# Performance work log

Hardware: AMD Instinct MI355X
Metric: run time of the kernel (lower is better)

Reference implementation:

```python
import jax, jax.numpy as jnp
import numpy as np

B, N_ST, N_SUB, WIN = 32, 8, 256, 2048


def setup_inputs() -> dict:
    key = jax.random.key(0)
    k1, k2 = jax.random.split(key)
    sel = jax.random.randint(k1, (B, WIN), 0, N_ST)
    schedule = jax.nn.one_hot(sel, N_ST, dtype=jnp.float32)
    # CSI: [B, n_stations, n_subcarriers, window]
    csi = jax.random.normal(k2, (B, N_ST, N_SUB, WIN), dtype=jnp.float32)
    return {"schedule": schedule, "csi": csi}


def reference(schedule, csi):
    # mask[b,t,s,w] = schedule[b,w,t]; out[b,s,w] = sum_t csi[b,t,s,w] * schedule[b,w,t]
    out = jnp.einsum('btsw,bwt->bsw', csi, schedule)
    return jnp.transpose(out, (0, 2, 1))
```

## Files before the change

kernel.cpp:

```cpp
#include <hip/hip_runtime.h>

constexpr int B     = 32;
constexpr int N_ST  = 8;
constexpr int N_SUB = 256;
constexpr int WIN   = 2048;

constexpr int TW  = 256;
constexpr int TS  = 16;
constexpr int STR = 260;

typedef float f4 __attribute__((ext_vector_type(4)));

__global__ __launch_bounds__(256)
void station_agg_kernel(const float* __restrict__ schedule,
                        const float* __restrict__ csi,
                        float* __restrict__ out)
{
    __shared__ float sched_t[N_ST][TW];
    __shared__ float tile2[TS * STR];

    const int s0 = blockIdx.x * TS;
    const int w0 = blockIdx.y * TW;
    const int b  = blockIdx.z;
    const int k  = threadIdx.x;
    const int wv = k >> 6;
    const int l  = k & 63;

    {
        const float* sp = schedule + ((size_t)b * WIN + w0 + k) * N_ST;
        const f4 a = *(const f4*)sp;
        const f4 c = *(const f4*)(sp + 4);
        sched_t[0][k] = a.x; sched_t[1][k] = a.y;
        sched_t[2][k] = a.z; sched_t[3][k] = a.w;
        sched_t[4][k] = c.x; sched_t[5][k] = c.y;
        sched_t[6][k] = c.z; sched_t[7][k] = c.w;
    }
    __syncthreads();

    f4 acc[4];
#pragma unroll
    for (int j = 0; j < 4; ++j) acc[j] = (f4)(0.0f);

    const size_t bbase = (size_t)b * N_ST * N_SUB * WIN;
#pragma unroll
    for (int t = 0; t < N_ST; ++t) {
        const f4 sv = *(const f4*)&sched_t[t][4 * l];
        const float* cp = csi + bbase
                        + ((size_t)t * N_SUB + (s0 + 4 * wv)) * WIN
                        + (w0 + 4 * l);
#pragma unroll
        for (int j = 0; j < 4; ++j) {
            const f4 c = __builtin_nontemporal_load((const f4*)(cp + (size_t)j * WIN));
            acc[j] += c * sv;
        }
    }

#pragma unroll
    for (int j = 0; j < 4; ++j)
        *(f4*)&tile2[(4 * wv + j) * STR + 4 * l] = acc[j];
    __syncthreads();

#pragma unroll
    for (int m = 0; m < 4; ++m) {
        const int wrow = 16 * wv + (l >> 2) + 64 * m;
        const int sl   = 4 * (l & 3);
        f4 o;
        o.x = tile2[(sl + 0) * STR + wrow];
        o.y = tile2[(sl + 1) * STR + wrow];
        o.z = tile2[(sl + 2) * STR + wrow];
        o.w = tile2[(sl + 3) * STR + wrow];
        __builtin_nontemporal_store(o,
            (f4*)(out + ((size_t)b * WIN + (w0 + wrow)) * N_SUB + (s0 + sl)));
    }
}

extern "C" void kernel_launch(void* const* d_in, const int* in_sizes, int n_in,
                              void* d_out, int out_size, void* d_ws, size_t ws_size,
                              hipStream_t stream) {
    const float* schedule = (const float*)d_in[0];
    const float* csi      = (const float*)d_in[1];
    float* out            = (float*)d_out;

    dim3 grid(N_SUB / TS, WIN / TW, B);
    dim3 block(256);
    station_agg_kernel<<<grid, block, 0, stream>>>(schedule, csi, out);
}
```

Baseline: 675.7 us.

## Batch CSI loads per half and drop LDS transpose for in-register stores

Groups the eight station loads into two batches of sixteen vector loads issued before any FMA, to raise memory-level parallelism. It also removes the shared-memory transpose tile and second barrier: each thread transposes its 4x4 accumulator block in registers and writes four 16-byte stores directly to the output. The cost is higher register pressure and less coalesced output writes, since each lane writes 16 bytes at stride N_SUB rather than forming contiguous rows across the wavefront. Output stores also change from nontemporal to regular.

```diff
diff --git a/kernel.cpp b/kernel.cpp
--- a/kernel.cpp
+++ b/kernel.cpp
@@ -7,7 +7,6 @@
 
 constexpr int TW  = 256;
 constexpr int TS  = 16;
-constexpr int STR = 260;
 
 typedef float f4 __attribute__((ext_vector_type(4)));
 
@@ -17,7 +16,6 @@
                         float* __restrict__ out)
 {
     __shared__ float sched_t[N_ST][TW];
-    __shared__ float tile2[TS * STR];
 
     const int s0 = blockIdx.x * TS;
     const int w0 = blockIdx.y * TW;
@@ -42,35 +40,45 @@
     for (int j = 0; j < 4; ++j) acc[j] = (f4)(0.0f);
 
     const size_t bbase = (size_t)b * N_ST * N_SUB * WIN;
+    const int    srow  = s0 + 4 * wv;
+    const int    wl    = w0 + 4 * l;
+
 #pragma unroll
-    for (int t = 0; t < N_ST; ++t) {
-        const f4 sv = *(const f4*)&sched_t[t][4 * l];
-        const float* cp = csi + bbase
-                        + ((size_t)t * N_SUB + (s0 + 4 * wv)) * WIN
-                        + (w0 + 4 * l);
+    for (int h = 0; h < 2; ++h) {
+        f4 cbuf[4][4];
+        f4 sv[4];
 #pragma unroll
-        for (int j = 0; j < 4; ++j) {
-            const f4 c = __builtin_nontemporal_load((const f4*)(cp + (size_t)j * WIN));
-            acc[j] += c * sv;
+        for (int tt = 0; tt < 4; ++tt) {
+            const int t = 4 * h + tt;
+            const float* cp = csi + bbase
+                            + ((size_t)t * N_SUB + srow) * WIN + wl;
+#pragma unroll
+            for (int j = 0; j < 4; ++j) {
+                cbuf[tt][j] = __builtin_nontemporal_load((const f4*)(cp + (size_t)j * WIN));
+            }
+        }
+#pragma unroll
+        for (int tt = 0; tt < 4; ++tt) {
+            sv[tt] = *(const f4*)&sched_t[4 * h + tt][4 * l];
+        }
+#pragma unroll
+        for (int tt = 0; tt < 4; ++tt) {
+#pragma unroll
+            for (int j = 0; j < 4; ++j) {
+                acc[j] += cbuf[tt][j] * sv[tt];
+            }
         }
     }
 
+    float* op = out + ((size_t)b * WIN + wl) * N_SUB + srow;
 #pragma unroll
-    for (int j = 0; j < 4; ++j)
-        *(f4*)&tile2[(4 * wv + j) * STR + 4 * l] = acc[j];
-    __syncthreads();
-
-#pragma unroll
-    for (int m = 0; m < 4; ++m) {
-        const int wrow = 16 * wv + (l >> 2) + 64 * m;
-        const int sl   = 4 * (l & 3);
+    for (int c = 0; c < 4; ++c) {
         f4 o;
-        o.x = tile2[(sl + 0) * STR + wrow];
-        o.y = tile2[(sl + 1) * STR + wrow];
-        o.z = tile2[(sl + 2) * STR + wrow];
-        o.w = tile2[(sl + 3) * STR + wrow];
-        __builtin_nontemporal_store(o,
-            (f4*)(out + ((size_t)b * WIN + (w0 + wrow)) * N_SUB + (s0 + sl)));
+        o.x = acc[0][c];
+        o.y = acc[1][c];
+        o.z = acc[2][c];
+        o.w = acc[3][c];
+        *(f4*)(op + (size_t)c * N_SUB) = o;
     }
 }
 
```

New measurement: 688.1 us. Within noise of the previous version (+1.8%).

## Double window tile, transpose in registers, drop LDS staging and nontemporal hints

Applied to the files above, without the earlier changes.

Each block now covers a 512-wide window tile, so every thread handles two column groups and loads twice as much CSI per iteration. The output transpose is now done in registers: each thread writes 16-byte rows of 4 subcarriers directly, with no shared-memory tile and no second barrier. Nontemporal load and store hints are replaced by plain accesses. The output writes become less coalesced (16 bytes per row with a 1 KB stride per thread), and the grid has half as many blocks.

```diff
diff --git a/kernel.cpp b/kernel.cpp
--- a/kernel.cpp
+++ b/kernel.cpp
@@ -5,9 +5,8 @@
 constexpr int N_SUB = 256;
 constexpr int WIN   = 2048;
 
-constexpr int TW  = 256;
+constexpr int TW  = 512;
 constexpr int TS  = 16;
-constexpr int STR = 260;
 
 typedef float f4 __attribute__((ext_vector_type(4)));
 
@@ -17,7 +16,6 @@
                         float* __restrict__ out)
 {
     __shared__ float sched_t[N_ST][TW];
-    __shared__ float tile2[TS * STR];
 
     const int s0 = blockIdx.x * TS;
     const int w0 = blockIdx.y * TW;
@@ -26,51 +24,56 @@
     const int wv = k >> 6;
     const int l  = k & 63;
 
-    {
-        const float* sp = schedule + ((size_t)b * WIN + w0 + k) * N_ST;
+#pragma unroll
+    for (int r = 0; r < 2; ++r) {
+        const int wr = k + 256 * r;
+        const float* sp = schedule + ((size_t)b * WIN + w0 + wr) * N_ST;
         const f4 a = *(const f4*)sp;
         const f4 c = *(const f4*)(sp + 4);
-        sched_t[0][k] = a.x; sched_t[1][k] = a.y;
-        sched_t[2][k] = a.z; sched_t[3][k] = a.w;
-        sched_t[4][k] = c.x; sched_t[5][k] = c.y;
-        sched_t[6][k] = c.z; sched_t[7][k] = c.w;
+        sched_t[0][wr] = a.x; sched_t[1][wr] = a.y;
+        sched_t[2][wr] = a.z; sched_t[3][wr] = a.w;
+        sched_t[4][wr] = c.x; sched_t[5][wr] = c.y;
+        sched_t[6][wr] = c.z; sched_t[7][wr] = c.w;
     }
     __syncthreads();
 
-    f4 acc[4];
+    f4 acc[2][4];
 #pragma unroll
-    for (int j = 0; j < 4; ++j) acc[j] = (f4)(0.0f);
+    for (int c = 0; c < 2; ++c)
+#pragma unroll
+        for (int j = 0; j < 4; ++j) acc[c][j] = (f4)(0.0f);
 
     const size_t bbase = (size_t)b * N_ST * N_SUB * WIN;
+    const int    srow  = s0 + 4 * wv;
+
 #pragma unroll
     for (int t = 0; t < N_ST; ++t) {
-        const f4 sv = *(const f4*)&sched_t[t][4 * l];
+        const f4 sv0 = *(const f4*)&sched_t[t][4 * l];
+        const f4 sv1 = *(const f4*)&sched_t[t][4 * l + 256];
         const float* cp = csi + bbase
-                        + ((size_t)t * N_SUB + (s0 + 4 * wv)) * WIN
-                        + (w0 + 4 * l);
+                        + ((size_t)t * N_SUB + srow) * WIN + (w0 + 4 * l);
 #pragma unroll
         for (int j = 0; j < 4; ++j) {
-            const f4 c = __builtin_nontemporal_load((const f4*)(cp + (size_t)j * WIN));
-            acc[j] += c * sv;
+            const f4 c0 = *(const f4*)(cp + (size_t)j * WIN);
+            const f4 c1 = *(const f4*)(cp + (size_t)j * WIN + 256);
+            acc[0][j] += c0 * sv0;
+            acc[1][j] += c1 * sv1;
         }
     }
 
 #pragma unroll
-    for (int j = 0; j < 4; ++j)
-        *(f4*)&tile2[(4 * wv + j) * STR + 4 * l] = acc[j];
-    __syncthreads();
-
+    for (int c = 0; c < 2; ++c) {
+        const int wbase = w0 + 4 * l + 256 * c;
+        float* op = out + ((size_t)b * WIN + wbase) * N_SUB + srow;
 #pragma unroll
-    for (int m = 0; m < 4; ++m) {
-        const int wrow = 16 * wv + (l >> 2) + 64 * m;
-        const int sl   = 4 * (l & 3);
-        f4 o;
-        o.x = tile2[(sl + 0) * STR + wrow];
-        o.y = tile2[(sl + 1) * STR + wrow];
-        o.z = tile2[(sl + 2) * STR + wrow];
-        o.w = tile2[(sl + 3) * STR + wrow];
-        __builtin_nontemporal_store(o,
-            (f4*)(out + ((size_t)b * WIN + (w0 + wrow)) * N_SUB + (s0 + sl)));
+        for (int col = 0; col < 4; ++col) {
+            f4 o;
+            o.x = acc[c][0][col];
+            o.y = acc[c][1][col];
+            o.z = acc[c][2][col];
+            o.w = acc[c][3][col];
+            *(f4*)(op + (size_t)col * N_SUB) = o;
+        }
     }
 }
 
```

Measured after the change: 715.3 us. 1.06x slower.
